# Performance work log

Hardware: AMD Instinct MI355X
Metric: run time of the kernel (lower is better)

Reference implementation:

```python
import jax, jax.numpy as jnp
import numpy as np

N_ENTITY = 100000
H_DIM = 512
N_ROWS = 262144
ALPHA = 0.5          # EMA rate for fast state
GATE_TH = 0.5        # gate_threshold buffer
GATE_SCALE = 5.0     # gate_scale buffer
LN_EPS = 1e-5


def setup_inputs() -> dict:
    key = jax.random.key(0)
    k1, k2, k3, k4, k5 = jax.random.split(key, 5)
    entity_emb = jax.random.normal(k1, (N_ROWS, H_DIM), dtype=jnp.float32)
    entity_ids = jax.random.randint(k2, (N_ROWS,), 0, N_ENTITY, dtype=jnp.int64)
    slow_state = 0.1 * jax.random.normal(k3, (N_ENTITY, H_DIM), dtype=jnp.float32)
    fast_state = 0.1 * jax.random.normal(k4, (N_ENTITY, H_DIM), dtype=jnp.float32)
    # torch nn.Linear(2h, h): weight shape (h, 2h), y = x @ W.T + b
    W = jax.random.normal(k5, (H_DIM, 2 * H_DIM), dtype=jnp.float32) * 0.02
    b = jnp.zeros((H_DIM,), dtype=jnp.float32)
    return {"entity_emb": entity_emb, "slow_state": slow_state,
            "fast_state": fast_state, "W": W, "b": b, "entity_ids": entity_ids}


def _layer_norm(x):
    mu = jnp.mean(x, axis=-1, keepdims=True)
    var = jnp.mean(jnp.square(x - mu), axis=-1, keepdims=True)
    return (x - mu) * jax.lax.rsqrt(var + LN_EPS)


def reference(entity_emb, slow_state, fast_state, W, b, entity_ids):
    # ---- fuse_with_state (gate path) ----
    state = slow_state[entity_ids]                                   # (N, h) gather
    is_active = (jnp.sum(jnp.abs(state), axis=-1, keepdims=True) > 1e-6).astype(entity_emb.dtype)
    h_state = _layer_norm(state)
    gate_in = jnp.concatenate([entity_emb, h_state], axis=-1)        # (N, 2h)
    z = jax.nn.sigmoid(gate_in @ W.T + b)                            # (N, h)
    fused = z * entity_emb + (1.0 - z) * h_state
    out = is_active * fused + (1.0 - is_active) * entity_emb

    # ---- writeback (no-grad in torch; scatter-reduce EMA + norm-gated slow update) ----
    ctx = jax.lax.stop_gradient(out)
    ids = entity_ids
    counts = jax.ops.segment_sum(jnp.ones((ctx.shape[0],), ctx.dtype), ids,
                                 num_segments=N_ENTITY)              # (E,)
    ctx_sum = jax.ops.segment_sum(ctx, ids, num_segments=N_ENTITY)   # (E, h)
    ctx_mean = ctx_sum / jnp.clip(counts, 1.0)[:, None]
    touched = (counts > 0)[:, None]
    new_fast_all = (1.0 - ALPHA) * fast_state + ALPHA * ctx_mean
    new_fast = jnp.where(touched, new_fast_all, fast_state)
    diff = new_fast - slow_state
    delta = jnp.linalg.norm(diff, axis=-1, keepdims=True)
    gate = jax.nn.sigmoid(GATE_SCALE * (delta - GATE_TH))
    new_slow = jnp.where(touched, slow_state + gate * diff, slow_state)
    return out, new_fast, new_slow
```

## Files before the change

kernel.cpp:

```cpp
#include <hip/hip_runtime.h>
#include <hip/hip_bf16.h>
#include <cstdint>

#define NROWS 262144
#define HDIM  512
#define NENT  100000
#define SCAN_NBLK ((NENT + 1023) / 1024)

typedef __attribute__((ext_vector_type(4))) float  f32x4;
typedef __attribute__((ext_vector_type(8))) short  bf16x8;
typedef __attribute__((ext_vector_type(4))) short  bf16x4;

static __device__ __forceinline__ unsigned short f2bf(float x) {
    unsigned u = __float_as_uint(x);
    u += 0x7FFF + ((u >> 16) & 1);
    return (unsigned short)(u >> 16);
}

static __device__ __forceinline__ void gll16(const void* g, void* l) {
    __builtin_amdgcn_global_load_lds(
        (const __attribute__((address_space(1))) unsigned int*)g,
        (__attribute__((address_space(3))) unsigned int*)l, 16, 0, 0);
}

__global__ void pack_w_kernel(const float* __restrict__ W, unsigned short* __restrict__ Wp) {
    int g    = blockIdx.x * 256 + threadIdx.x;
    int lane = g & 63;
    int nt   = (g >> 6) & 31;
    int kt   = g >> 11;
    int col  = nt * 16 + (lane & 15);
    int k    = kt * 32 + ((lane >> 4) << 3);
    const float* src = W + (size_t)col * 1024 + k;
    f32x4 v0 = *(const f32x4*)(src);
    f32x4 v1 = *(const f32x4*)(src + 4);
    bf16x8 ov;
#pragma unroll
    for (int i = 0; i < 4; ++i) {
        ov[i]     = (short)f2bf(v0[i]);
        ov[4 + i] = (short)f2bf(v1[i]);
    }
    *(bf16x8*)(Wp + (size_t)g * 8) = ov;
}

__global__ __launch_bounds__(256) void count_kernel(const int* __restrict__ ids,
                                                    unsigned* __restrict__ counts) {
    int r = blockIdx.x * 256 + threadIdx.x;
    if (r < NROWS) atomicAdd(&counts[ids[r]], 1u);
}

__global__ __launch_bounds__(1024) void scan1_kernel(const unsigned* __restrict__ counts,
                                                     unsigned* __restrict__ off,
                                                     unsigned* __restrict__ bsums) {
    __shared__ unsigned tmp[1024];
    int i = blockIdx.x * 1024 + threadIdx.x;
    unsigned v = (i < NENT) ? counts[i] : 0u;
    tmp[threadIdx.x] = v;
    __syncthreads();
#pragma unroll
    for (int o = 1; o < 1024; o <<= 1) {
        unsigned a = (threadIdx.x >= o) ? tmp[threadIdx.x - o] : 0u;
        __syncthreads();
        tmp[threadIdx.x] += a;
        __syncthreads();
    }
    if (i < NENT) off[i] = tmp[threadIdx.x] - v;
    if (threadIdx.x == 1023) bsums[blockIdx.x] = tmp[1023];
}

__global__ void scan2_kernel(unsigned* __restrict__ bsums) {
    if (threadIdx.x == 0 && blockIdx.x == 0) {
        unsigned s = 0;
        for (int i = 0; i < SCAN_NBLK; ++i) { unsigned t = bsums[i]; bsums[i] = s; s += t; }
    }
}

__global__ __launch_bounds__(1024) void scan3_kernel(unsigned* __restrict__ off,
                                                     const unsigned* __restrict__ bsums,
                                                     unsigned* __restrict__ cursor) {
    int i = blockIdx.x * 1024 + threadIdx.x;
    if (i < NENT) {
        unsigned o = off[i] + bsums[blockIdx.x];
        off[i] = o;
        cursor[i] = o;
    }
    if (i == 0) off[NENT] = NROWS;
}

__global__ __launch_bounds__(256) void fill_kernel(const int* __restrict__ ids,
                                                   unsigned* __restrict__ cursor,
                                                   int* __restrict__ rowidx) {
    int r = blockIdx.x * 256 + threadIdx.x;
    if (r < NROWS) {
        unsigned p = atomicAdd(&cursor[ids[r]], 1u);
        rowidx[p] = r;
    }
}

__global__ __launch_bounds__(512, 4) void fuse_kernel(
    const float* __restrict__ emb, const float* __restrict__ slow,
    const unsigned short* __restrict__ Wp, const float* __restrict__ bias,
    const int* __restrict__ ids, float* __restrict__ out)
{
    __shared__ unsigned short wT[2048 * 8];
    __shared__ unsigned short xT[2][256 * 8];
    __shared__ float muS[64], rsS[64], actS[64], bS[512];
    __shared__ int idS[64];

    const int t    = threadIdx.x;
    const int w    = t >> 6;
    const int lane = t & 63;
    const int brow = blockIdx.x * 64;

    if (t < 128) ((f32x4*)bS)[t] = ((const f32x4*)bias)[t];

    for (int rr = 0; rr < 8; ++rr) {
        int row = w * 8 + rr;
        int id  = ids[brow + row];
        const float* sp = slow + (size_t)id * HDIM;
        f32x4 v0 = ((const f32x4*)sp)[lane * 2];
        f32x4 v1 = ((const f32x4*)sp)[lane * 2 + 1];
        float s = 0.f, s2 = 0.f, sa = 0.f;
#pragma unroll
        for (int i = 0; i < 4; ++i) {
            s  += v0[i] + v1[i];
            s2 += v0[i] * v0[i] + v1[i] * v1[i];
            sa += fabsf(v0[i]) + fabsf(v1[i]);
        }
#pragma unroll
        for (int m = 32; m >= 1; m >>= 1) {
            s  += __shfl_xor(s, m);
            s2 += __shfl_xor(s2, m);
            sa += __shfl_xor(sa, m);
        }
        if (lane == 0) {
            float mu  = s * (1.f / HDIM);
            float var = s2 * (1.f / HDIM) - mu * mu;
            muS[row]  = mu;
            rsS[row]  = rsqrtf(var + 1e-5f);
            actS[row] = (sa > 1e-6f) ? 1.f : 0.f;
            idS[row]  = id;
        }
    }
    __syncthreads();

    const int xrow = t >> 3;
    const int k4   = (t & 7) * 4;
    const float* srcSt = slow + (size_t)idS[xrow] * HDIM + k4;
    const float* srcEm = emb + (size_t)(brow + xrow) * HDIM + k4;
    const float muR = muS[xrow], rsR = rsS[xrow];
    const int xByte = (((xrow >> 4) * 64 + (((k4 >> 3) << 4) | (xrow & 15))) << 4) + ((k4 & 7) << 1);

    f32x4 zero4 = {0.f, 0.f, 0.f, 0.f};
    f32x4 acc[4][4];
#pragma unroll
    for (int i = 0; i < 4; ++i)
#pragma unroll
        for (int j = 0; j < 4; ++j) acc[i][j] = zero4;

#define LOAD_X(ph, xr)                                                   \
    {   const float* p = ((ph) < 16) ? (srcSt + (ph) * 32)               \
                                     : (srcEm + ((ph) - 16) * 32);       \
        xr = *(const f32x4*)p;                                           \
    }

    f32x4 xr;
    LOAD_X(0, xr);

    for (int ph = 0; ph < 32; ++ph) {
        const int cur = ph & 1;
        if (ph) __syncthreads();

        {
            f32x4 y = xr;
            if (ph < 16) {
#pragma unroll
                for (int i = 0; i < 4; ++i) y[i] = (y[i] - muR) * rsR;
            }
            bf16x4 xv;
#pragma unroll
            for (int i = 0; i < 4; ++i) xv[i] = (short)f2bf(y[i]);
            *(bf16x4*)((char*)xT[cur] + xByte) = xv;
        }
        {
            const int ktW = (ph < 16) ? (16 + ph) : (ph - 16);
            const unsigned short* wsrc = Wp + (size_t)ktW * 16384;
#pragma unroll
            for (int i = 0; i < 4; ++i)
                gll16(wsrc + (size_t)(i * 512 + t) * 8,
                      (char*)wT + i * 8192 + w * 1024 + lane * 16);
        }
        __syncthreads();

        if (ph < 31) LOAD_X(ph + 1, xr);

        bf16x8 wf0 = *(const bf16x8*)((char*)wT + ((w * 4 + 0) * 64 + lane) * 16);
        bf16x8 wf1 = *(const bf16x8*)((char*)wT + ((w * 4 + 1) * 64 + lane) * 16);
        bf16x8 wf2 = *(const bf16x8*)((char*)wT + ((w * 4 + 2) * 64 + lane) * 16);
        bf16x8 wf3 = *(const bf16x8*)((char*)wT + ((w * 4 + 3) * 64 + lane) * 16);
#pragma unroll
        for (int rt = 0; rt < 4; ++rt) {
            bf16x8 xf = *(const bf16x8*)((char*)xT[cur] + ((rt * 64 + lane) * 16));
            acc[rt][0] = __builtin_amdgcn_mfma_f32_16x16x32_bf16(wf0, xf, acc[rt][0], 0, 0, 0);
            acc[rt][1] = __builtin_amdgcn_mfma_f32_16x16x32_bf16(wf1, xf, acc[rt][1], 0, 0, 0);
            acc[rt][2] = __builtin_amdgcn_mfma_f32_16x16x32_bf16(wf2, xf, acc[rt][2], 0, 0, 0);
            acc[rt][3] = __builtin_amdgcn_mfma_f32_16x16x32_bf16(wf3, xf, acc[rt][3], 0, 0, 0);
        }
    }
#undef LOAD_X

#pragma unroll
    for (int rt = 0; rt < 4; ++rt) {
        int rowl = rt * 16 + (lane & 15);
        int grow = brow + rowl;
        int id   = idS[rowl];
        float mu = muS[rowl], rs = rsS[rowl], act = actS[rowl];
        const float* embP  = emb  + (size_t)grow * HDIM;
        const float* slowP = slow + (size_t)id * HDIM;
        float*       outP  = out  + (size_t)grow * HDIM;
#pragma unroll
        for (int ct = 0; ct < 4; ++ct) {
            int col0 = w * 64 + ct * 16 + ((lane >> 4) << 2);
            f32x4 bv = *(const f32x4*)&bS[col0];
            f32x4 ev = *(const f32x4*)(embP + col0);
            f32x4 sv = *(const f32x4*)(slowP + col0);
            f32x4 o;
#pragma unroll
            for (int r = 0; r < 4; ++r) {
                float logit = acc[rt][ct][r] + bv[r];
                float z  = 1.f / (1.f + __expf(-logit));
                float h  = (sv[r] - mu) * rs;
                float fused = z * ev[r] + (1.f - z) * h;
                o[r] = (act > 0.f) ? fused : ev[r];
            }
            *(f32x4*)(outP + col0) = o;
        }
    }
}

__global__ __launch_bounds__(256) void finalize_kernel(
    const float* __restrict__ fast, const float* __restrict__ slow,
    const float* __restrict__ out, const unsigned* __restrict__ off,
    const int* __restrict__ rowidx, float* __restrict__ nf, float* __restrict__ ns)
{
    int e = blockIdx.x * 4 + (threadIdx.x >> 6);
    if (e >= NENT) return;
    int lane = threadIdx.x & 63;
    size_t base = (size_t)e * HDIM + lane * 8;

    f32x4 f0 = *(const f32x4*)(fast + base), f1 = *(const f32x4*)(fast + base + 4);
    f32x4 l0 = *(const f32x4*)(slow + base), l1 = *(const f32x4*)(slow + base + 4);

    unsigned o0 = off[e], o1 = off[e + 1];
    int c = (int)(o1 - o0);

    if (c == 0) {
        *(f32x4*)(nf + base)     = f0;
        *(f32x4*)(nf + base + 4) = f1;
        *(f32x4*)(ns + base)     = l0;
        *(f32x4*)(ns + base + 4) = l1;
        return;
    }

    f32x4 s0 = {0.f, 0.f, 0.f, 0.f}, s1 = {0.f, 0.f, 0.f, 0.f};
    for (int j = 0; j < c; ++j) {
        int r = rowidx[o0 + j];
        const float* p = out + (size_t)r * HDIM + lane * 8;
        s0 += *(const f32x4*)p;
        s1 += *(const f32x4*)(p + 4);
    }

    float inv = 0.5f / (float)c;
    f32x4 n0, n1, d0, d1;
    float ss = 0.f;
#pragma unroll
    for (int i = 0; i < 4; ++i) {
        n0[i] = 0.5f * f0[i] + s0[i] * inv;
        n1[i] = 0.5f * f1[i] + s1[i] * inv;
        d0[i] = n0[i] - l0[i]; ss += d0[i] * d0[i];
        d1[i] = n1[i] - l1[i]; ss += d1[i] * d1[i];
    }
#pragma unroll
    for (int m = 32; m >= 1; m >>= 1) ss += __shfl_xor(ss, m);
    float delta = sqrtf(ss);
    float gate  = 1.f / (1.f + expf(-5.f * (delta - 0.5f)));

    f32x4 o0v, o1v;
#pragma unroll
    for (int i = 0; i < 4; ++i) {
        o0v[i] = l0[i] + gate * d0[i];
        o1v[i] = l1[i] + gate * d1[i];
    }
    *(f32x4*)(nf + base)     = n0;
    *(f32x4*)(nf + base + 4) = n1;
    *(f32x4*)(ns + base)     = o0v;
    *(f32x4*)(ns + base + 4) = o1v;
}

extern "C" void kernel_launch(void* const* d_in, const int* in_sizes, int n_in,
                              void* d_out, int out_size, void* d_ws, size_t ws_size,
                              hipStream_t stream) {
    const float* emb  = (const float*)d_in[0];
    const float* slow = (const float*)d_in[1];
    const float* fast = (const float*)d_in[2];
    const float* W    = (const float*)d_in[3];
    const float* bias = (const float*)d_in[4];
    const int*   ids  = (const int*)d_in[5];

    float* out = (float*)d_out;
    float* nf  = out + (size_t)NROWS * HDIM;
    float* ns  = nf + (size_t)NENT * HDIM;

    unsigned short* Wp   = (unsigned short*)d_ws;
    unsigned* counts     = (unsigned*)((char*)d_ws + (1u << 20));
    unsigned* off        = (unsigned*)((char*)d_ws + (1u << 20) + 512 * 1024);
    unsigned* bsums      = (unsigned*)((char*)d_ws + (2u << 20));
    int*      rowidx     = (int*)((char*)d_ws + (2u << 20) + 4096);

    hipMemsetAsync(counts, 0, (size_t)NENT * sizeof(unsigned), stream);

    pack_w_kernel<<<256, 256, 0, stream>>>(W, Wp);
    count_kernel<<<NROWS / 256, 256, 0, stream>>>(ids, counts);
    scan1_kernel<<<SCAN_NBLK, 1024, 0, stream>>>(counts, off, bsums);
    scan2_kernel<<<1, 64, 0, stream>>>(bsums);
    scan3_kernel<<<SCAN_NBLK, 1024, 0, stream>>>(off, bsums, counts);
    fill_kernel<<<NROWS / 256, 256, 0, stream>>>(ids, counts, rowidx);
    fuse_kernel<<<NROWS / 64, 512, 0, stream>>>(emb, slow, Wp, bias, ids, out);
    finalize_kernel<<<(NENT + 3) / 4, 256, 0, stream>>>(fast, slow, out, off, rowidx, nf, ns);
}
```

Measured before the change: 1.029 ms.

## Double-buffer W tiles in LDS and prefetch activations two phases ahead

```diff
diff --git a/kernel.cpp b/kernel.cpp
--- a/kernel.cpp
+++ b/kernel.cpp
@@ -101,7 +101,7 @@
     const unsigned short* __restrict__ Wp, const float* __restrict__ bias,
     const int* __restrict__ ids, float* __restrict__ out)
 {
-    __shared__ unsigned short wT[2048 * 8];
+    __shared__ unsigned short wT[2][2048 * 8];
     __shared__ unsigned short xT[2][256 * 8];
     __shared__ float muS[64], rsS[64], actS[64], bS[512];
     __shared__ int idS[64];
@@ -162,41 +162,42 @@
                                      : (srcEm + ((ph) - 16) * 32);       \
         xr = *(const f32x4*)p;                                           \
     }
-
-    f32x4 xr;
-    LOAD_X(0, xr);
+#define PACK_X(ph, xr, buf)                                              \
+    {   f32x4 y = xr;                                                    \
+        if ((ph) < 16) {                                                 \
+            _Pragma("unroll")                                            \
+            for (int i = 0; i < 4; ++i) y[i] = (y[i] - muR) * rsR;       \
+        }                                                                \
+        bf16x4 xv;                                                       \
+        _Pragma("unroll")                                                \
+        for (int i = 0; i < 4; ++i) xv[i] = (short)f2bf(y[i]);           \
+        *(bf16x4*)((char*)xT[buf] + xByte) = xv;                         \
+    }
+#define GLL_W(ph, buf)                                                   \
+    {   const int ktW = ((ph) < 16) ? (16 + (ph)) : ((ph) - 16);         \
+        const unsigned short* wsrc = Wp + (size_t)ktW * 16384;           \
+        _Pragma("unroll")                                                \
+        for (int i = 0; i < 4; ++i)                                      \
+            gll16(wsrc + (size_t)(i * 512 + t) * 8,                      \
+                  (char*)wT[buf] + i * 8192 + w * 1024 + lane * 16);     \
+    }
+
+    f32x4 xA, xB;
+    GLL_W(0, 0);
+    {   f32x4 x0; LOAD_X(0, x0); PACK_X(0, x0, 0); }
+    LOAD_X(1, xA);
+    __syncthreads();
 
     for (int ph = 0; ph < 32; ++ph) {
-        const int cur = ph & 1;
-        if (ph) __syncthreads();
-
-        {
-            f32x4 y = xr;
-            if (ph < 16) {
-#pragma unroll
-                for (int i = 0; i < 4; ++i) y[i] = (y[i] - muR) * rsR;
-            }
-            bf16x4 xv;
-#pragma unroll
-            for (int i = 0; i < 4; ++i) xv[i] = (short)f2bf(y[i]);
-            *(bf16x4*)((char*)xT[cur] + xByte) = xv;
-        }
-        {
-            const int ktW = (ph < 16) ? (16 + ph) : (ph - 16);
-            const unsigned short* wsrc = Wp + (size_t)ktW * 16384;
-#pragma unroll
-            for (int i = 0; i < 4; ++i)
-                gll16(wsrc + (size_t)(i * 512 + t) * 8,
-                      (char*)wT + i * 8192 + w * 1024 + lane * 16);
-        }
-        __syncthreads();
-
-        if (ph < 31) LOAD_X(ph + 1, xr);
-
-        bf16x8 wf0 = *(const bf16x8*)((char*)wT + ((w * 4 + 0) * 64 + lane) * 16);
-        bf16x8 wf1 = *(const bf16x8*)((char*)wT + ((w * 4 + 1) * 64 + lane) * 16);
-        bf16x8 wf2 = *(const bf16x8*)((char*)wT + ((w * 4 + 2) * 64 + lane) * 16);
-        bf16x8 wf3 = *(const bf16x8*)((char*)wT + ((w * 4 + 3) * 64 + lane) * 16);
+        const int cur = ph & 1, nxt = cur ^ 1;
+
+        if (ph < 31) GLL_W(ph + 1, nxt);
+        if (ph < 30) LOAD_X(ph + 2, xB);
+
+        bf16x8 wf0 = *(const bf16x8*)((char*)wT[cur] + ((w * 4 + 0) * 64 + lane) * 16);
+        bf16x8 wf1 = *(const bf16x8*)((char*)wT[cur] + ((w * 4 + 1) * 64 + lane) * 16);
+        bf16x8 wf2 = *(const bf16x8*)((char*)wT[cur] + ((w * 4 + 2) * 64 + lane) * 16);
+        bf16x8 wf3 = *(const bf16x8*)((char*)wT[cur] + ((w * 4 + 3) * 64 + lane) * 16);
 #pragma unroll
         for (int rt = 0; rt < 4; ++rt) {
             bf16x8 xf = *(const bf16x8*)((char*)xT[cur] + ((rt * 64 + lane) * 16));
@@ -205,8 +206,14 @@
             acc[rt][2] = __builtin_amdgcn_mfma_f32_16x16x32_bf16(wf2, xf, acc[rt][2], 0, 0, 0);
             acc[rt][3] = __builtin_amdgcn_mfma_f32_16x16x32_bf16(wf3, xf, acc[rt][3], 0, 0, 0);
         }
+
+        if (ph < 31) PACK_X(ph + 1, xA, nxt);
+        xA = xB;
+        __syncthreads();
     }
 #undef LOAD_X
+#undef PACK_X
+#undef GLL_W
 
 #pragma unroll
     for (int rt = 0; rt < 4; ++rt) {
```

After: 989.1 us. -3.9%, faster.
